# Performance work log

Hardware: AMD Instinct MI355X
Metric: run time of the kernel (lower is better)

## Reference

```python
import math
import jax, jax.numpy as jnp
import numpy as np

D_MODEL = 128
NUM_HEADS = 8
FACTOR = 5


def setup_inputs() -> dict:
    key = jax.random.key(0)
    ks = jax.random.split(key, 9)
    B, L, dm = 2, 4096, D_MODEL
    s = 1.0 / math.sqrt(dm)
    return {
        "x": jax.random.normal(ks[0], (B, L, dm), dtype=jnp.float32),
        "Wq": jax.random.normal(ks[1], (dm, dm), dtype=jnp.float32) * s,
        "bq": jnp.zeros((dm,), jnp.float32),
        "Wk": jax.random.normal(ks[2], (dm, dm), dtype=jnp.float32) * s,
        "bk": jnp.zeros((dm,), jnp.float32),
        "Wv": jax.random.normal(ks[3], (dm, dm), dtype=jnp.float32) * s,
        "bv": jnp.zeros((dm,), jnp.float32),
        "Wo": jax.random.normal(ks[4], (dm, dm), dtype=jnp.float32) * s,
        "bo": jnp.zeros((dm,), jnp.float32),
    }


def reference(x, Wq, bq, Wk, bk, Wv, bv, Wo, bo):
    B, L, dm = x.shape
    H = NUM_HEADS
    D = dm // H
    inv_sqrt_d = 1.0 / math.sqrt(D)

    def split_heads(t):  # [B,L,dm] -> [B,H,L,D]
        return t.reshape(B, L, H, D).transpose(0, 2, 1, 3)

    Q = split_heads(x @ Wq + bq)
    K = split_heads(x @ Wk + bk)
    V = split_heads(x @ Wv + bv)

    # sample_k = min(L_K, int(log(L_K) * factor)); L is static under jit
    sample_k = min(L, int(math.log(L) * FACTOR))

    # _prob_QK: full scores, per-query stable exp, mean over queries, top-k keys
    scores_full = jnp.einsum("bhqd,bhkd->bhqk", Q, K) * inv_sqrt_d  # [B,H,L,L]
    m = jnp.max(scores_full, axis=-1, keepdims=True)
    e = jnp.exp(scores_full - m)
    mean_attn = jnp.mean(e, axis=2)  # [B,H,L_K]
    _, idx = jax.lax.top_k(mean_attn, sample_k)  # [B,H,sample_k]

    # gather sampled keys/values along the key axis
    Ks = jnp.take_along_axis(K, idx[..., None], axis=2)  # [B,H,s,D]
    Vs = jnp.take_along_axis(V, idx[..., None], axis=2)

    attn = jax.nn.softmax(jnp.einsum("bhqd,bhsd->bhqs", Q, Ks) * inv_sqrt_d, axis=-1)
    out = jnp.einsum("bhqs,bhsd->bhqd", attn, Vs)  # [B,H,L,D]
    out = out.transpose(0, 2, 1, 3).reshape(B, L, dm)
    return out @ Wo + bo
```

## Files before the change

### kernel.cpp

```cpp
#include <hip/hip_runtime.h>
#include <hip/hip_bf16.h>

#define L 4096
#define DM 128
#define NH 8
#define HD 16
#define NBH 16
#define SK 41
#define NSPLIT 16
#define KCH (32/NSPLIT)
#define QSCALE 0.36067376022224085f

typedef __attribute__((ext_vector_type(8))) short s16x8;
typedef __attribute__((ext_vector_type(4))) float f32x4;

__device__ __forceinline__ float bf2f(unsigned short h){ return __uint_as_float(((unsigned)h)<<16); }
__device__ __forceinline__ unsigned short f2bf(float f){
  unsigned u = __float_as_uint(f);
  u += 0x7FFFu + ((u>>16)&1u);
  return (unsigned short)(u>>16);
}
__device__ __forceinline__ float fast_exp2(float x){
  float r;
  asm("v_exp_f32 %0, %1" : "=v"(r) : "v"(x));
  return r;
}

__global__ __launch_bounds__(256) void prep(
    const float* __restrict__ x,
    const float* __restrict__ Wq, const float* __restrict__ Wk,
    const float* __restrict__ Wv, const float* __restrict__ Wo,
    unsigned short* __restrict__ Xh, unsigned short* __restrict__ Xl,
    unsigned short* __restrict__ Wph, unsigned short* __restrict__ Wpl)
{
  const int t = threadIdx.x;
  const int blk = blockIdx.x;
  if (blk < 1024){
    const long base = (long)blk*1024 + t*4;
    float4 v = *(const float4*)(x + base);
    unsigned short h[4], lo[4];
    h[0]=f2bf(v.x); lo[0]=f2bf(v.x - bf2f(h[0]));
    h[1]=f2bf(v.y); lo[1]=f2bf(v.y - bf2f(h[1]));
    h[2]=f2bf(v.z); lo[2]=f2bf(v.z - bf2f(h[2]));
    h[3]=f2bf(v.w); lo[3]=f2bf(v.w - bf2f(h[3]));
    *(uint2*)(Xh+base) = *(uint2*)h;
    *(uint2*)(Xl+base) = *(uint2*)lo;
  } else {
    const int e = (blk-1024)*256 + t;
    const int p = e >> 14;
    const int idx = e & 16383;
    const int j = idx & 7;
    const int f = idx >> 3;
    const int n = f & 127;
    const int kcg = f >> 7;
    const int k = (kcg>>1)*16 + (kcg&1)*8 + j;
    const float* W = (p==0)?Wq:((p==1)?Wk:((p==2)?Wv:Wo));
    const float v = W[k*128 + n];
    const unsigned short h = f2bf(v);
    Wph[e] = h;
    Wpl[e] = f2bf(v - bf2f(h));
  }
}

__global__ __launch_bounds__(256) void proj_mfma(
    const unsigned short* __restrict__ Xh, const unsigned short* __restrict__ Xl,
    const unsigned short* __restrict__ Wph, const unsigned short* __restrict__ Wpl,
    const float* __restrict__ bq, const float* __restrict__ bk, const float* __restrict__ bv,
    unsigned short* __restrict__ Qh, unsigned short* __restrict__ Ql,
    unsigned short* __restrict__ Kh, unsigned short* __restrict__ Kl,
    float* __restrict__ Vo)
{
  const int p = blockIdx.y;
  const float* __restrict__ bias = (p==0)?bq:((p==1)?bk:bv);
  __shared__ __align__(16) unsigned short wh[16384];
  __shared__ __align__(16) unsigned short wl[16384];
  const int t = threadIdx.x;
  {
    const uint4* gh = (const uint4*)(Wph + (long)p*16384);
    const uint4* gl = (const uint4*)(Wpl + (long)p*16384);
    uint4* sh = (uint4*)wh; uint4* sl = (uint4*)wl;
#pragma unroll
    for (int i=0;i<8;++i){ sh[t + i*256] = gh[t + i*256]; sl[t + i*256] = gl[t + i*256]; }
  }
  __syncthreads();
  const int w = t>>6, l = t&63;
  const int lc = l&15, g = l>>4;
  const int mbase = blockIdx.x*256 + w*64;
  f32x4 acc[4][8];
#pragma unroll
  for (int mt=0;mt<4;++mt)
#pragma unroll
    for (int nt=0;nt<8;++nt){ acc[mt][nt][0]=0.f; acc[mt][nt][1]=0.f; acc[mt][nt][2]=0.f; acc[mt][nt][3]=0.f; }
  const unsigned short* __restrict__ Asrc = (g<2)? Xh : Xl;
  const int koff = (g&1)*8;
  for (int kc=0; kc<8; ++kc){
    s16x8 a[4];
#pragma unroll
    for (int mt=0;mt<4;++mt)
      a[mt] = *(const s16x8*)(Asrc + ((long)(mbase + mt*16 + lc))*128 + kc*16 + koff);
#pragma unroll
    for (int nt=0;nt<8;++nt){
      const int fi = (kc*2+(g&1))*128 + nt*16 + lc;
      s16x8 b1 = ((const s16x8*)wh)[fi];
      s16x8 b2 = ((const s16x8*)wl)[fi];
#pragma unroll
      for (int mt=0;mt<4;++mt){
        acc[mt][nt] = __builtin_amdgcn_mfma_f32_16x16x32_bf16(a[mt], b1, acc[mt][nt], 0,0,0);
        acc[mt][nt] = __builtin_amdgcn_mfma_f32_16x16x32_bf16(a[mt], b2, acc[mt][nt], 0,0,0);
      }
    }
  }
#pragma unroll
  for (int nt=0;nt<8;++nt){
    const float bb = bias[nt*16 + lc];
#pragma unroll
    for (int mt=0;mt<4;++mt){
#pragma unroll
      for (int r=0;r<4;++r){
        const int row = mbase + mt*16 + g*4 + r;
        float v = acc[mt][nt][r] + bb;
        const int b = row>>12, li = row&4095;
        const long o = (((long)(b*NH + nt))*L + li)*HD + lc;
        if (p==2){
          Vo[o] = v;
        } else {
          if (p==0) v *= QSCALE;
          const unsigned short h = f2bf(v);
          const unsigned short lo2 = f2bf(v - bf2f(h));
          if (p==0){ Qh[o]=h; Ql[o]=lo2; } else { Kh[o]=h; Kl[o]=lo2; }
        }
      }
    }
  }
}

__global__ __launch_bounds__(256) void rowmax_k(
    const unsigned short* __restrict__ Qh, const unsigned short* __restrict__ Ql,
    const unsigned short* __restrict__ Kh, const unsigned short* __restrict__ Kl,
    float* __restrict__ mpart)
{
  const int bh = blockIdx.y, qt = blockIdx.x, ks = blockIdx.z;
  const int t = threadIdx.x, w = t>>6, l = t&63;
  const int half = (l>>4)&1, part = l>>5, lc = l&15;
  __shared__ __align__(16) unsigned short khs[2048];
  __shared__ __align__(16) unsigned short kls[2048];
  s16x8 aq[4];
  {
    const unsigned short* Qsrc = part ? Ql : Qh;
#pragma unroll
    for (int m=0;m<4;++m){
      const int row = qt*256 + w*64 + m*16 + lc;
      aq[m] = *(const s16x8*)(Qsrc + (((long)bh*L + row)*HD) + half*8);
    }
  }
  f32x4 fz; fz[0]=0.f; fz[1]=0.f; fz[2]=0.f; fz[3]=0.f;
  f32x4 rmax[4];
#pragma unroll
  for (int m=0;m<4;++m){ rmax[m][0]=rmax[m][1]=rmax[m][2]=rmax[m][3]=-3.4e38f; }
  const s16x8* khg = (const s16x8*)(Kh + (long)bh*L*HD);
  const s16x8* klg = (const s16x8*)(Kl + (long)bh*L*HD);
  const int c0 = ks*KCH;
  s16x8 pk = khg[c0*256 + t], pl = klg[c0*256 + t];
  for (int kc=0; kc<KCH; ++kc){
    __syncthreads();
    ((s16x8*)khs)[t] = pk;
    ((s16x8*)kls)[t] = pl;
    if (kc+1 < KCH){ pk = khg[(c0+kc+1)*256 + t]; pl = klg[(c0+kc+1)*256 + t]; }
    __syncthreads();
#pragma unroll
    for (int s=0;s<8;++s){
      const int key = s*16 + lc;
      s16x8 b1 = ((const s16x8*)khs)[key*2 + half];
      s16x8 b2 = ((const s16x8*)kls)[key*2 + half];
#pragma unroll
      for (int m=0;m<4;++m){
        f32x4 acc = __builtin_amdgcn_mfma_f32_16x16x32_bf16(aq[m], b2, fz, 0,0,0);
        acc = __builtin_amdgcn_mfma_f32_16x16x32_bf16(aq[m], b1, acc, 0,0,0);
#pragma unroll
        for (int r=0;r<4;++r) rmax[m][r] = fmaxf(rmax[m][r], acc[r]);
      }
    }
  }
#pragma unroll
  for (int m=0;m<4;++m){
#pragma unroll
    for (int r=0;r<4;++r){
      float v = rmax[m][r];
      v = fmaxf(v, __shfl_xor(v, 1));
      v = fmaxf(v, __shfl_xor(v, 2));
      v = fmaxf(v, __shfl_xor(v, 4));
      v = fmaxf(v, __shfl_xor(v, 8));
      rmax[m][r] = v;
    }
  }
  if (lc == 0){
    const int q4 = l>>4;
#pragma unroll
    for (int m=0;m<4;++m){
#pragma unroll
      for (int r=0;r<4;++r){
        const int row = qt*256 + w*64 + m*16 + q4*4 + r;
        mpart[((long)ks*NBH + bh)*L + row] = rmax[m][r];
      }
    }
  }
}

__global__ __launch_bounds__(256) void mreduce(
    const float* __restrict__ mpart, float* __restrict__ wq)
{
  const int i = blockIdx.x*256 + threadIdx.x;
  float m = -3.4e38f;
#pragma unroll
  for (int p=0;p<NSPLIT;++p) m = fmaxf(m, mpart[(long)p*NBH*L + i]);
  wq[i] = fast_exp2(-m);
}

__global__ __launch_bounds__(256) void colexp_k(
    const unsigned short* __restrict__ Kh, const unsigned short* __restrict__ Kl,
    const unsigned short* __restrict__ Qh, const unsigned short* __restrict__ Ql,
    const float* __restrict__ wq, float* __restrict__ cspart)
{
  const int bh = blockIdx.y, kt = blockIdx.x, qs = blockIdx.z;
  const int t = threadIdx.x, w = t>>6, l = t&63;
  const int half = (l>>4)&1, part = l>>5, lc = l&15;
  __shared__ __align__(16) unsigned short qhs[2048];
  __shared__ __align__(16) unsigned short qls[2048];
  __shared__ float ws[128];
  s16x8 ak[4];
  {
    const unsigned short* Ksrc = part ? Kl : Kh;
#pragma unroll
    for (int m=0;m<4;++m){
      const int key = kt*256 + w*64 + m*16 + lc;
      ak[m] = *(const s16x8*)(Ksrc + (((long)bh*L + key)*HD) + half*8);
    }
  }
  f32x4 fz; fz[0]=0.f; fz[1]=0.f; fz[2]=0.f; fz[3]=0.f;
  f32x4 csum[4];
#pragma unroll
  for (int m=0;m<4;++m){ csum[m][0]=0.f; csum[m][1]=0.f; csum[m][2]=0.f; csum[m][3]=0.f; }
  const s16x8* qhg = (const s16x8*)(Qh + (long)bh*L*HD);
  const s16x8* qlg = (const s16x8*)(Ql + (long)bh*L*HD);
  const float* wg = wq + (long)bh*L;
  const int c0 = qs*KCH;
  s16x8 pk = qhg[c0*256 + t], pl = qlg[c0*256 + t];
  float pw = (t<128) ? wg[c0*128 + t] : 0.f;
  for (int qc=0; qc<KCH; ++qc){
    __syncthreads();
    ((s16x8*)qhs)[t] = pk;
    ((s16x8*)qls)[t] = pl;
    if (t < 128) ws[t] = pw;
    if (qc+1 < KCH){
      pk = qhg[(c0+qc+1)*256 + t]; pl = qlg[(c0+qc+1)*256 + t];
      if (t < 128) pw = wg[(c0+qc+1)*128 + t];
    }
    __syncthreads();
#pragma unroll
    for (int s=0;s<8;++s){
      const int qq = s*16 + lc;
      s16x8 b1 = ((const s16x8*)qhs)[qq*2 + half];
      s16x8 b2 = ((const s16x8*)qls)[qq*2 + half];
      const float wv = ws[s*16 + lc];
#pragma unroll
      for (int m=0;m<4;++m){
        f32x4 acc = __builtin_amdgcn_mfma_f32_16x16x32_bf16(ak[m], b2, fz, 0,0,0);
        acc = __builtin_amdgcn_mfma_f32_16x16x32_bf16(ak[m], b1, acc, 0,0,0);
#pragma unroll
        for (int r=0;r<4;++r)
          csum[m][r] = fmaf(fast_exp2(acc[r]), wv, csum[m][r]);
      }
    }
  }
#pragma unroll
  for (int m=0;m<4;++m){
#pragma unroll
    for (int r=0;r<4;++r){
      float v = csum[m][r];
      v += __shfl_xor(v, 1);
      v += __shfl_xor(v, 2);
      v += __shfl_xor(v, 4);
      v += __shfl_xor(v, 8);
      csum[m][r] = v;
    }
  }
  if (lc == 0){
    const int k4 = l>>4;
#pragma unroll
    for (int m=0;m<4;++m){
#pragma unroll
      for (int r=0;r<4;++r){
        const int key = kt*256 + w*64 + m*16 + k4*4 + r;
        cspart[((long)qs*NBH + bh)*L + key] = csum[m][r];
      }
    }
  }
}

__global__ __launch_bounds__(256) void csreduce(
    const float* __restrict__ cspart, float* __restrict__ cs)
{
  const int gid = blockIdx.x*256 + threadIdx.x;
  const long i4 = (long)gid*4;
  float4 s = {0.f,0.f,0.f,0.f};
#pragma unroll
  for (int p=0;p<NSPLIT;++p){
    float4 v = *(const float4*)(cspart + (long)p*NBH*L + i4);
    s.x += v.x; s.y += v.y; s.z += v.z; s.w += v.w;
  }
  *(float4*)(cs + i4) = s;
}

__global__ __launch_bounds__(256) void topk_gather(
    const float* __restrict__ cs,
    const unsigned short* __restrict__ Kh, const unsigned short* __restrict__ Kl,
    const float* __restrict__ V,
    float* __restrict__ Ks, float* __restrict__ Vs)
{
  const int bh = blockIdx.x;
  const int t = threadIdx.x;
  __shared__ float vals[4096];
  __shared__ unsigned hist[2048];
  __shared__ unsigned suf[256];
  __shared__ int meta[4];
  __shared__ int sel[SK];
  __shared__ int sorted[SK];
  __shared__ int tiei[4096];

  for (int i=t; i<1024; i+=256)
    *(float4*)&vals[i*4] = *(const float4*)(cs + (long)bh*L + i*4);
  __syncthreads();

  int target = SK;
  unsigned B1 = 0, P2 = 0, T = 0;
#pragma unroll
  for (int pass=0; pass<3; ++pass){
    const int nb = (pass<2) ? 2048 : 1024;
    const int chunk = nb >> 8;
    for (int i=t;i<nb;i+=256) hist[i]=0u;
    __syncthreads();
    for (int i=t;i<4096;i+=256){
      const unsigned u = __float_as_uint(vals[i]);
      bool ok; int bk;
      if (pass==0){ ok = true;              bk = (int)(u>>21); }
      else if (pass==1){ ok = ((u>>21)==B1); bk = (int)((u>>10)&0x7FFu); }
      else { ok = ((u>>10)==P2);            bk = (int)(u&0x3FFu); }
      if (ok) atomicAdd(&hist[bk], 1u);
    }
    __syncthreads();
    {
      unsigned c=0;
#pragma unroll
      for (int b=0;b<8;++b) if (b<chunk) c += hist[t*chunk+b];
      suf[t]=c;
    }
    __syncthreads();
    for (int off=1; off<256; off<<=1){
      unsigned add = (t+off<256)? suf[t+off] : 0u;
      __syncthreads();
      suf[t] += add;
      __syncthreads();
    }
    {
      const unsigned mysuf = suf[t];
      const unsigned nxt = (t==255)?0u:suf[t+1];
      if (mysuf >= (unsigned)target && nxt < (unsigned)target){
        unsigned running = nxt;
        for (int b=t*chunk+chunk-1; b>=t*chunk; --b){
          const unsigned h = hist[b];
          if (running + h >= (unsigned)target){ meta[0]=b; meta[1]=(int)running; break; }
          running += h;
        }
      }
    }
    __syncthreads();
    const unsigned B = (unsigned)meta[0];
    target -= meta[1];
    if (pass==0) B1 = B;
    else if (pass==1) P2 = (B1<<11)|B;
    else T = (P2<<10)|B;
    __syncthreads();
  }
  if (t==0){ meta[2]=0; meta[3]=0; }
  __syncthreads();
  for (int i=t;i<4096;i+=256){
    const unsigned u = __float_as_uint(vals[i]);
    if (u > T){ int p = atomicAdd(&meta[2],1); sel[p]=i; }
    else if (u == T){ int p = atomicAdd(&meta[3],1); tiei[p]=i; }
  }
  __syncthreads();
  const int ngt = meta[2];
  const int ntie = meta[3];
  for (int j=t; j<ntie; j+=256){
    const int x = tiei[j];
    int rk=0;
    for (int k=0;k<ntie;++k) rk += (tiei[k] < x);
    if (rk < target) sel[ngt+rk] = x;
  }
  __syncthreads();
  if (t<SK){
    int x=sel[t]; int rk=0;
    for (int j=0;j<SK;++j) rk += (sel[j]<x);
    sorted[rk]=x;
  }
  __syncthreads();
  for (int i=t;i<SK*HD;i+=256){
    const int j=i>>4, dd=i&15;
    const int key=sorted[j];
    const long src=((long)bh*L+key)*HD+dd;
    Ks[(long)bh*SK*HD+i]=bf2f(Kh[src])+bf2f(Kl[src]);
    Vs[(long)bh*SK*HD+i]=V[src];
  }
}

__global__ __launch_bounds__(256) void sattn(
    const unsigned short* __restrict__ Qh, const unsigned short* __restrict__ Ql,
    const float* __restrict__ Ks, const float* __restrict__ Vs,
    unsigned short* __restrict__ AOh, unsigned short* __restrict__ AOl)
{
  const int bh = blockIdx.y, qb = blockIdx.x;
  const int t = threadIdx.x;
  __shared__ float ks[SK*HD], vs[SK*HD];
  for (int i=t; i<SK*HD; i+=256){
    ks[i] = Ks[(long)bh*SK*HD + i];
    vs[i] = Vs[(long)bh*SK*HD + i];
  }
  __syncthreads();
  const int q = qb*256 + t;
  const long qo = ((long)bh*L + q)*HD;
  float qv[16];
  {
    s16x8 h0 = *(const s16x8*)(Qh+qo);
    s16x8 h1 = *(const s16x8*)(Qh+qo+8);
    s16x8 l0 = *(const s16x8*)(Ql+qo);
    s16x8 l1 = *(const s16x8*)(Ql+qo+8);
#pragma unroll
    for (int d=0; d<8; ++d){
      qv[d]   = bf2f((unsigned short)h0[d]) + bf2f((unsigned short)l0[d]);
      qv[d+8] = bf2f((unsigned short)h1[d]) + bf2f((unsigned short)l1[d]);
    }
  }
  float mrun = -3.4e38f, lrun = 0.f, out[16];
#pragma unroll
  for (int d=0; d<16; ++d) out[d] = 0.f;
  for (int j=0; j<SK; ++j){
    float s = 0.f;
#pragma unroll
    for (int d=0; d<16; ++d) s = fmaf(qv[d], ks[j*HD+d], s);
    if (s > mrun){
      const float c = fast_exp2(mrun - s);
      lrun *= c;
#pragma unroll
      for (int d=0; d<16; ++d) out[d] *= c;
      mrun = s;
    }
    const float p = fast_exp2(s - mrun);
    lrun += p;
#pragma unroll
    for (int d=0; d<16; ++d) out[d] = fmaf(p, vs[j*HD+d], out[d]);
  }
  const float inv = 1.f / lrun;
  const int b = bh>>3, h = bh&7;
  const long row = (long)b*L + q;
  unsigned short hv[16], lv[16];
#pragma unroll
  for (int d=0; d<16; ++d){
    const float v = out[d]*inv;
    hv[d] = f2bf(v);
    lv[d] = f2bf(v - bf2f(hv[d]));
  }
  unsigned short* oh = AOh + row*DM + h*HD;
  unsigned short* ol = AOl + row*DM + h*HD;
  *(uint4*)(oh)   = *(uint4*)(hv);
  *(uint4*)(oh+8) = *(uint4*)(hv+8);
  *(uint4*)(ol)   = *(uint4*)(lv);
  *(uint4*)(ol+8) = *(uint4*)(lv+8);
}

__global__ __launch_bounds__(256) void outproj_mfma(
    const unsigned short* __restrict__ AOh, const unsigned short* __restrict__ AOl,
    const unsigned short* __restrict__ Wph, const unsigned short* __restrict__ Wpl,
    const float* __restrict__ bo, float* __restrict__ out)
{
  __shared__ __align__(16) unsigned short wh[16384];
  __shared__ __align__(16) unsigned short wl[16384];
  const int t = threadIdx.x;
  {
    const uint4* gh = (const uint4*)(Wph + (long)3*16384);
    const uint4* gl = (const uint4*)(Wpl + (long)3*16384);
    uint4* sh = (uint4*)wh; uint4* sl = (uint4*)wl;
#pragma unroll
    for (int i=0;i<8;++i){ sh[t + i*256] = gh[t + i*256]; sl[t + i*256] = gl[t + i*256]; }
  }
  __syncthreads();
  const int w = t>>6, l = t&63;
  const int lc = l&15, g = l>>4;
  const int mbase = blockIdx.x*256 + w*64;
  f32x4 acc[4][8];
#pragma unroll
  for (int mt=0;mt<4;++mt)
#pragma unroll
    for (int nt=0;nt<8;++nt){ acc[mt][nt][0]=0.f; acc[mt][nt][1]=0.f; acc[mt][nt][2]=0.f; acc[mt][nt][3]=0.f; }
  const unsigned short* __restrict__ Asrc = (g<2)? AOh : AOl;
  const int koff = (g&1)*8;
  for (int kc=0; kc<8; ++kc){
    s16x8 a[4];
#pragma unroll
    for (int mt=0;mt<4;++mt)
      a[mt] = *(const s16x8*)(Asrc + ((long)(mbase + mt*16 + lc))*128 + kc*16 + koff);
#pragma unroll
    for (int nt=0;nt<8;++nt){
      const int fi = (kc*2+(g&1))*128 + nt*16 + lc;
      s16x8 b1 = ((const s16x8*)wh)[fi];
      s16x8 b2 = ((const s16x8*)wl)[fi];
#pragma unroll
      for (int mt=0;mt<4;++mt){
        acc[mt][nt] = __builtin_amdgcn_mfma_f32_16x16x32_bf16(a[mt], b1, acc[mt][nt], 0,0,0);
        acc[mt][nt] = __builtin_amdgcn_mfma_f32_16x16x32_bf16(a[mt], b2, acc[mt][nt], 0,0,0);
      }
    }
  }
#pragma unroll
  for (int nt=0;nt<8;++nt){
    const float bb = bo[nt*16 + lc];
#pragma unroll
    for (int mt=0;mt<4;++mt){
#pragma unroll
      for (int r=0;r<4;++r){
        const int row = mbase + mt*16 + g*4 + r;
        out[(long)row*DM + nt*16 + lc] = acc[mt][nt][r] + bb;
      }
    }
  }
}

extern "C" void kernel_launch(void* const* d_in, const int* in_sizes, int n_in,
                              void* d_out, int out_size, void* d_ws, size_t ws_size,
                              hipStream_t stream)
{
  const float* x  = (const float*)d_in[0];
  const float* Wq = (const float*)d_in[1];
  const float* bq = (const float*)d_in[2];
  const float* Wk = (const float*)d_in[3];
  const float* bk = (const float*)d_in[4];
  const float* Wv = (const float*)d_in[5];
  const float* bv = (const float*)d_in[6];
  const float* Wo = (const float*)d_in[7];
  const float* bo = (const float*)d_in[8];
  float* out = (float*)d_out;

  char* wsp = (char*)d_ws;
  size_t o = 0;
  auto alloc = [&](size_t bytes)->char*{
    char* p = wsp + o; o += (bytes + 255) & ~(size_t)255; return p;
  };
  unsigned short* Qh = (unsigned short*)alloc((size_t)NBH*L*HD*2);
  unsigned short* Ql = (unsigned short*)alloc((size_t)NBH*L*HD*2);
  unsigned short* Kh = (unsigned short*)alloc((size_t)NBH*L*HD*2);
  unsigned short* Kl = (unsigned short*)alloc((size_t)NBH*L*HD*2);
  float* Vv    = (float*)alloc((size_t)NBH*L*HD*4);
  float* mpart = (float*)alloc((size_t)NSPLIT*NBH*L*4);
  float* cspart= (float*)alloc((size_t)NSPLIT*NBH*L*4);
  float* csv   = (float*)alloc((size_t)NBH*L*4);
  float* wqv   = (float*)alloc((size_t)NBH*L*4);
  float* Ks    = (float*)alloc((size_t)NBH*SK*HD*4);
  float* Vs    = (float*)alloc((size_t)NBH*SK*HD*4);
  unsigned short* Xh  = (unsigned short*)alloc((size_t)2*L*DM*2);
  unsigned short* Xl  = (unsigned short*)alloc((size_t)2*L*DM*2);
  unsigned short* AOh = (unsigned short*)alloc((size_t)2*L*DM*2);
  unsigned short* AOl = (unsigned short*)alloc((size_t)2*L*DM*2);
  unsigned short* Wph = (unsigned short*)alloc((size_t)4*16384*2);
  unsigned short* Wpl = (unsigned short*)alloc((size_t)4*16384*2);

  prep<<<1280,256,0,stream>>>(x,Wq,Wk,Wv,Wo,Xh,Xl,Wph,Wpl);
  proj_mfma<<<dim3(32,3),256,0,stream>>>(Xh,Xl,Wph,Wpl,bq,bk,bv,Qh,Ql,Kh,Kl,Vv);
  rowmax_k<<<dim3(16,16,NSPLIT),256,0,stream>>>(Qh,Ql,Kh,Kl,mpart);
  mreduce<<<NBH*L/256,256,0,stream>>>(mpart,wqv);
  colexp_k<<<dim3(16,16,NSPLIT),256,0,stream>>>(Kh,Kl,Qh,Ql,wqv,cspart);
  csreduce<<<NBH*L/1024,256,0,stream>>>(cspart,csv);
  topk_gather<<<16,256,0,stream>>>(csv,Kh,Kl,Vv,Ks,Vs);
  sattn<<<dim3(16,16),256,0,stream>>>(Qh,Ql,Ks,Vs,AOh,AOl);
  outproj_mfma<<<32,256,0,stream>>>(AOh,AOl,Wph,Wpl,bo,out);
}
```

Baseline: 161.4 us.

## Stream K/Q tiles directly from global memory, drop LDS staging, reduce split count

The rowmax and column-exp kernels no longer stage 128-row tiles into shared memory behind two barriers per chunk. Each lane now loads its 16-key (or 16-query) fragment straight from global memory with a one-step register prefetch. The split count falls from 16 to 4, so each block covers 1024 keys or queries instead of 256, giving fewer, longer blocks and fewer partial maxima and sums to reduce. The sparse attention kernel also reads sampled K and V from shared memory as float4 vectors. The risks are exposed global-load latency without LDS reuse and lower grid parallelism.

Result: no change. 160.2 us (-0.8%).

```diff
diff --git a/kernel.cpp b/kernel.cpp
--- a/kernel.cpp
+++ b/kernel.cpp
@@ -7,8 +7,7 @@
 #define HD 16
 #define NBH 16
 #define SK 41
-#define NSPLIT 16
-#define KCH (32/NSPLIT)
+#define NSPLIT 4
 #define QSCALE 0.36067376022224085f
 
 typedef __attribute__((ext_vector_type(8))) short s16x8;
@@ -142,8 +141,6 @@
   const int bh = blockIdx.y, qt = blockIdx.x, ks = blockIdx.z;
   const int t = threadIdx.x, w = t>>6, l = t&63;
   const int half = (l>>4)&1, part = l>>5, lc = l&15;
-  __shared__ __align__(16) unsigned short khs[2048];
-  __shared__ __align__(16) unsigned short kls[2048];
   s16x8 aq[4];
   {
     const unsigned short* Qsrc = part ? Ql : Qh;
@@ -157,28 +154,22 @@
   f32x4 rmax[4];
 #pragma unroll
   for (int m=0;m<4;++m){ rmax[m][0]=rmax[m][1]=rmax[m][2]=rmax[m][3]=-3.4e38f; }
-  const s16x8* khg = (const s16x8*)(Kh + (long)bh*L*HD);
-  const s16x8* klg = (const s16x8*)(Kl + (long)bh*L*HD);
-  const int c0 = ks*KCH;
-  s16x8 pk = khg[c0*256 + t], pl = klg[c0*256 + t];
-  for (int kc=0; kc<KCH; ++kc){
-    __syncthreads();
-    ((s16x8*)khs)[t] = pk;
-    ((s16x8*)kls)[t] = pl;
-    if (kc+1 < KCH){ pk = khg[(c0+kc+1)*256 + t]; pl = klg[(c0+kc+1)*256 + t]; }
-    __syncthreads();
-#pragma unroll
-    for (int s=0;s<8;++s){
-      const int key = s*16 + lc;
-      s16x8 b1 = ((const s16x8*)khs)[key*2 + half];
-      s16x8 b2 = ((const s16x8*)kls)[key*2 + half];
-#pragma unroll
-      for (int m=0;m<4;++m){
-        f32x4 acc = __builtin_amdgcn_mfma_f32_16x16x32_bf16(aq[m], b2, fz, 0,0,0);
-        acc = __builtin_amdgcn_mfma_f32_16x16x32_bf16(aq[m], b1, acc, 0,0,0);
-#pragma unroll
-        for (int r=0;r<4;++r) rmax[m][r] = fmaxf(rmax[m][r], acc[r]);
-      }
+  const unsigned short* khp = Kh + ((long)bh*L + ks*1024 + lc)*HD + half*8;
+  const unsigned short* klp = Kl + ((long)bh*L + ks*1024 + lc)*HD + half*8;
+  s16x8 nb1 = *(const s16x8*)khp;
+  s16x8 nb2 = *(const s16x8*)klp;
+  for (int kk=0; kk<64; ++kk){
+    s16x8 b1 = nb1, b2 = nb2;
+    if (kk < 63){
+      nb1 = *(const s16x8*)(khp + (kk+1)*16*HD);
+      nb2 = *(const s16x8*)(klp + (kk+1)*16*HD);
+    }
+#pragma unroll
+    for (int m=0;m<4;++m){
+      f32x4 acc = __builtin_amdgcn_mfma_f32_16x16x32_bf16(aq[m], b2, fz, 0,0,0);
+      acc = __builtin_amdgcn_mfma_f32_16x16x32_bf16(aq[m], b1, acc, 0,0,0);
+#pragma unroll
+      for (int r=0;r<4;++r) rmax[m][r] = fmaxf(rmax[m][r], acc[r]);
     }
   }
 #pragma unroll
@@ -224,9 +215,6 @@
   const int bh = blockIdx.y, kt = blockIdx.x, qs = blockIdx.z;
   const int t = threadIdx.x, w = t>>6, l = t&63;
   const int half = (l>>4)&1, part = l>>5, lc = l&15;
-  __shared__ __align__(16) unsigned short qhs[2048];
-  __shared__ __align__(16) unsigned short qls[2048];
-  __shared__ float ws[128];
   s16x8 ak[4];
   {
     const unsigned short* Ksrc = part ? Kl : Kh;
@@ -240,36 +228,27 @@
   f32x4 csum[4];
 #pragma unroll
   for (int m=0;m<4;++m){ csum[m][0]=0.f; csum[m][1]=0.f; csum[m][2]=0.f; csum[m][3]=0.f; }
-  const s16x8* qhg = (const s16x8*)(Qh + (long)bh*L*HD);
-  const s16x8* qlg = (const s16x8*)(Ql + (long)bh*L*HD);
-  const float* wg = wq + (long)bh*L;
-  const int c0 = qs*KCH;
-  s16x8 pk = qhg[c0*256 + t], pl = qlg[c0*256 + t];
-  float pw = (t<128) ? wg[c0*128 + t] : 0.f;
-  for (int qc=0; qc<KCH; ++qc){
-    __syncthreads();
-    ((s16x8*)qhs)[t] = pk;
-    ((s16x8*)qls)[t] = pl;
-    if (t < 128) ws[t] = pw;
-    if (qc+1 < KCH){
-      pk = qhg[(c0+qc+1)*256 + t]; pl = qlg[(c0+qc+1)*256 + t];
-      if (t < 128) pw = wg[(c0+qc+1)*128 + t];
-    }
-    __syncthreads();
-#pragma unroll
-    for (int s=0;s<8;++s){
-      const int qq = s*16 + lc;
-      s16x8 b1 = ((const s16x8*)qhs)[qq*2 + half];
-      s16x8 b2 = ((const s16x8*)qls)[qq*2 + half];
-      const float wv = ws[s*16 + lc];
-#pragma unroll
-      for (int m=0;m<4;++m){
-        f32x4 acc = __builtin_amdgcn_mfma_f32_16x16x32_bf16(ak[m], b2, fz, 0,0,0);
-        acc = __builtin_amdgcn_mfma_f32_16x16x32_bf16(ak[m], b1, acc, 0,0,0);
-#pragma unroll
-        for (int r=0;r<4;++r)
-          csum[m][r] = fmaf(fast_exp2(acc[r]), wv, csum[m][r]);
-      }
+  const unsigned short* qhp = Qh + ((long)bh*L + qs*1024 + lc)*HD + half*8;
+  const unsigned short* qlp = Ql + ((long)bh*L + qs*1024 + lc)*HD + half*8;
+  const float* wg = wq + (long)bh*L + qs*1024 + lc;
+  s16x8 nb1 = *(const s16x8*)qhp;
+  s16x8 nb2 = *(const s16x8*)qlp;
+  float nw = *wg;
+  for (int kk=0; kk<64; ++kk){
+    s16x8 b1 = nb1, b2 = nb2;
+    const float wv = nw;
+    if (kk < 63){
+      nb1 = *(const s16x8*)(qhp + (kk+1)*16*HD);
+      nb2 = *(const s16x8*)(qlp + (kk+1)*16*HD);
+      nw  = wg[(kk+1)*16];
+    }
+#pragma unroll
+    for (int m=0;m<4;++m){
+      f32x4 acc = __builtin_amdgcn_mfma_f32_16x16x32_bf16(ak[m], b2, fz, 0,0,0);
+      acc = __builtin_amdgcn_mfma_f32_16x16x32_bf16(ak[m], b1, acc, 0,0,0);
+#pragma unroll
+      for (int r=0;r<4;++r)
+        csum[m][r] = fmaf(fast_exp2(acc[r]), wv, csum[m][r]);
     }
   }
 #pragma unroll
@@ -444,9 +423,15 @@
 #pragma unroll
   for (int d=0; d<16; ++d) out[d] = 0.f;
   for (int j=0; j<SK; ++j){
-    float s = 0.f;
-#pragma unroll
-    for (int d=0; d<16; ++d) s = fmaf(qv[d], ks[j*HD+d], s);
+    float4 k0 = *(const float4*)&ks[j*HD+0];
+    float4 k1 = *(const float4*)&ks[j*HD+4];
+    float4 k2 = *(const float4*)&ks[j*HD+8];
+    float4 k3 = *(const float4*)&ks[j*HD+12];
+    float s = qv[0]*k0.x;
+    s = fmaf(qv[1],k0.y,s); s = fmaf(qv[2],k0.z,s); s = fmaf(qv[3],k0.w,s);
+    s = fmaf(qv[4],k1.x,s); s = fmaf(qv[5],k1.y,s); s = fmaf(qv[6],k1.z,s); s = fmaf(qv[7],k1.w,s);
+    s = fmaf(qv[8],k2.x,s); s = fmaf(qv[9],k2.y,s); s = fmaf(qv[10],k2.z,s); s = fmaf(qv[11],k2.w,s);
+    s = fmaf(qv[12],k3.x,s); s = fmaf(qv[13],k3.y,s); s = fmaf(qv[14],k3.z,s); s = fmaf(qv[15],k3.w,s);
     if (s > mrun){
       const float c = fast_exp2(mrun - s);
       lrun *= c;
@@ -456,8 +441,14 @@
     }
     const float p = fast_exp2(s - mrun);
     lrun += p;
-#pragma unroll
-    for (int d=0; d<16; ++d) out[d] = fmaf(p, vs[j*HD+d], out[d]);
+    float4 v0 = *(const float4*)&vs[j*HD+0];
+    float4 v1 = *(const float4*)&vs[j*HD+4];
+    float4 v2 = *(const float4*)&vs[j*HD+8];
+    float4 v3 = *(const float4*)&vs[j*HD+12];
+    out[0]=fmaf(p,v0.x,out[0]); out[1]=fmaf(p,v0.y,out[1]); out[2]=fmaf(p,v0.z,out[2]); out[3]=fmaf(p,v0.w,out[3]);
+    out[4]=fmaf(p,v1.x,out[4]); out[5]=fmaf(p,v1.y,out[5]); out[6]=fmaf(p,v1.z,out[6]); out[7]=fmaf(p,v1.w,out[7]);
+    out[8]=fmaf(p,v2.x,out[8]); out[9]=fmaf(p,v2.y,out[9]); out[10]=fmaf(p,v2.z,out[10]); out[11]=fmaf(p,v2.w,out[11]);
+    out[12]=fmaf(p,v3.x,out[12]); out[13]=fmaf(p,v3.y,out[13]); out[14]=fmaf(p,v3.z,out[14]); out[15]=fmaf(p,v3.w,out[15]);
   }
   const float inv = 1.f / lrun;
   const int b = bh>>3, h = bh&7;
```
